# Kernel tuning notes

Hardware: AMD Instinct MI355X
Metric: run time of the kernel (lower is better)

## Reference

```python
import jax, jax.numpy as jnp
import numpy as np

N_HEAD = 16

def _rope_tables(T, hd, dtype):
    inv_freq = 1.0 / (10000.0 ** (jnp.arange(0, hd, 2, dtype=jnp.float32) / hd))
    t = jnp.arange(T, dtype=jnp.float32)
    freqs = jnp.outer(t, inv_freq)                 # [T, hd/2]
    emb = jnp.concatenate([freqs, freqs], axis=-1)  # [T, hd]
    return jnp.cos(emb).astype(dtype), jnp.sin(emb).astype(dtype)

def _rotate_half(x):
    x1, x2 = jnp.split(x, 2, axis=-1)
    return jnp.concatenate([-x2, x1], axis=-1)

def setup_inputs() -> dict:
    key = jax.random.key(0)
    ks = jax.random.split(key, 3)
    B, T, C = 2, 2048, 1024
    x = jax.random.normal(ks[0], (B, T, C), dtype=jnp.float32)
    W_attn = jax.random.normal(ks[1], (C, 3 * C), dtype=jnp.float32) * 0.02
    b_attn = jnp.zeros((3 * C,), dtype=jnp.float32)
    W_proj = jax.random.normal(ks[2], (C, C), dtype=jnp.float32) * 0.02
    b_proj = jnp.zeros((C,), dtype=jnp.float32)
    return {"x": x, "W_attn": W_attn, "b_attn": b_attn, "W_proj": W_proj, "b_proj": b_proj}

def reference(x, W_attn, b_attn, W_proj, b_proj):
    B, T, C = x.shape
    H = N_HEAD
    hd = C // H
    qkv = x @ W_attn + b_attn                       # [B,T,3C]
    q, k, v = jnp.split(qkv, 3, axis=-1)
    # [B,T,C] -> [B,H,T,hd]
    to_heads = lambda a: a.reshape(B, T, H, hd).transpose(0, 2, 1, 3)
    q, k, v = to_heads(q), to_heads(k), to_heads(v)
    cos, sin = _rope_tables(T, hd, x.dtype)         # [T,hd]
    q = q * cos + _rotate_half(q) * sin
    k = k * cos + _rotate_half(k) * sin
    scale = 1.0 / jnp.sqrt(jnp.asarray(hd, dtype=x.dtype))
    scores = jnp.einsum('bhqd,bhkd->bhqk', q, k) * scale
    causal = jnp.tril(jnp.ones((T, T), dtype=bool))
    scores = jnp.where(causal, scores, jnp.finfo(x.dtype).min)
    attn = jax.nn.softmax(scores, axis=-1)
    y = jnp.einsum('bhqk,bhkd->bhqd', attn, v)      # [B,H,T,hd]
    y = y.transpose(0, 2, 1, 3).reshape(B, T, C)
    return y @ W_proj + b_proj
```

## Files before the change

kernel.cpp:

```cpp
#include <hip/hip_runtime.h>
#include <math.h>

#define B_  2
#define T_  2048
#define C_  1024
#define H_  16
#define HD_ 64

typedef __bf16 bf16x8 __attribute__((ext_vector_type(8)));
typedef float  f32x4  __attribute__((ext_vector_type(4)));

__device__ __forceinline__ unsigned short f2bf(float f) {
    unsigned int u = __float_as_uint(f);
    unsigned int r = (u + 0x7fffu + ((u >> 16) & 1u)) >> 16;
    return (unsigned short)r;
}

__device__ __forceinline__ void async16(const void* g, void* l) {
    __builtin_amdgcn_global_load_lds(
        (const __attribute__((address_space(1))) unsigned int*)g,
        (__attribute__((address_space(3))) unsigned int*)l, 16, 0, 0);
}

__global__ __launch_bounds__(256)
void castk(const float* __restrict__ in, unsigned short* __restrict__ out, int n4)
{
    const int i = blockIdx.x * 256 + threadIdx.x;
    if (i >= n4) return;
    const float4 v = ((const float4*)in)[i];
    ushort4 o;
    o.x = f2bf(v.x); o.y = f2bf(v.y); o.z = f2bf(v.z); o.w = f2bf(v.w);
    ((ushort4*)out)[i] = o;
}

__global__ __launch_bounds__(256)
void transcast_k(const float* __restrict__ in, unsigned short* __restrict__ out,
                 int K, int N)
{
    __shared__ float t[32][33];
    const int n0 = blockIdx.x * 32, k0 = blockIdx.y * 32;
    const int tx = threadIdx.x & 31, ty = threadIdx.x >> 5;
    #pragma unroll
    for (int r = 0; r < 4; ++r)
        t[ty + 8 * r][tx] = in[(size_t)(k0 + ty + 8 * r) * N + n0 + tx];
    __syncthreads();
    #pragma unroll
    for (int r = 0; r < 4; ++r)
        out[(size_t)(n0 + ty + 8 * r) * K + k0 + tx] = f2bf(t[tx][ty + 8 * r]);
}

__global__ __launch_bounds__(256)
void rope_table_k(float2* __restrict__ tab)
{
    const int idx = blockIdx.x * 256 + threadIdx.x;
    const int dd = idx & 31;
    const int t  = idx >> 5;
    const float invf = expf(-(float)dd * (9.210340371976184f / 32.0f));
    float sn, cs;
    sincosf((float)t * invf, &sn, &cs);
    tab[idx] = make_float2(cs, sn);
}

template<int MODE>
__global__ __launch_bounds__(256)
void mgemm(const unsigned short* __restrict__ A, const unsigned short* __restrict__ Bt,
           const float* __restrict__ bias, const float2* __restrict__ rope,
           void* __restrict__ out0, void* __restrict__ out1, void* __restrict__ out2,
           int M, int N, int K)
{
    __shared__ __align__(16) unsigned short As[128 * 32];
    __shared__ __align__(16) unsigned short Bs[128 * 32];

    const int tid  = threadIdx.x;
    const int lane = tid & 63;
    const int wid  = tid >> 6;
    const int m0 = blockIdx.y * 128;
    const int n0 = blockIdx.x * 128;
    const int wr = wid >> 1, wc = wid & 1;

    const int srow = wid * 32 + (lane >> 2);
    const int scol = (lane & 3) * 8;
    const unsigned short* gA = A  + (size_t)(m0 + srow) * K + scol;
    const unsigned short* gB = Bt + (size_t)(n0 + srow) * K + scol;
    unsigned short* lA = As + wid * 1024;
    unsigned short* lB = Bs + wid * 1024;

    f32x4 acc[4][4];
    #pragma unroll
    for (int i = 0; i < 4; ++i)
        #pragma unroll
        for (int j = 0; j < 4; ++j) acc[i][j] = (f32x4)0.f;

    const int r15 = lane & 15;
    const int ko  = (lane >> 4) * 8;

    for (int kt = 0; kt < K; kt += 32) {
        __syncthreads();
        async16(gA + kt,          lA);
        async16(gA + kt + 16 * K, lA + 512);
        async16(gB + kt,          lB);
        async16(gB + kt + 16 * K, lB + 512);
        __syncthreads();

        bf16x8 af[4], bg[4];
        #pragma unroll
        for (int i = 0; i < 4; ++i)
            af[i] = *(const bf16x8*)(As + (wr * 64 + i * 16 + r15) * 32 + ko);
        #pragma unroll
        for (int j = 0; j < 4; ++j)
            bg[j] = *(const bf16x8*)(Bs + (wc * 64 + j * 16 + r15) * 32 + ko);
        #pragma unroll
        for (int i = 0; i < 4; ++i)
            #pragma unroll
            for (int j = 0; j < 4; ++j)
                acc[i][j] = __builtin_amdgcn_mfma_f32_16x16x32_bf16(af[i], bg[j], acc[i][j], 0, 0, 0);
    }

    const int rg = (lane >> 4) * 4;
    if (MODE == 0) {
        const int which = n0 >> 10;
        if (which < 2) {
            unsigned short* dst = (unsigned short*)(which == 0 ? out0 : out1);
            const int h = ((n0 & 1023) >> 6) + wc;
            #pragma unroll
            for (int i = 0; i < 4; ++i) {
                #pragma unroll
                for (int r = 0; r < 4; ++r) {
                    const int row = m0 + wr * 64 + i * 16 + rg + r;
                    const int b = row >> 11, t = row & 2047;
                    const size_t obase = (((size_t)(b * H_ + h)) * T_ + t) * HD_;
                    #pragma unroll
                    for (int j = 0; j < 2; ++j) {
                        const int d1 = j * 16 + r15;
                        const float v1 = acc[i][j][r]     + bias[n0 + wc * 64 + d1];
                        const float v2 = acc[i][j + 2][r] + bias[n0 + wc * 64 + d1 + 32];
                        const float2 cssn = rope[t * 32 + d1];
                        dst[obase + d1]      = f2bf(v1 * cssn.x - v2 * cssn.y);
                        dst[obase + d1 + 32] = f2bf(v2 * cssn.x + v1 * cssn.y);
                    }
                }
            }
        } else {
            #pragma unroll
            for (int j = 0; j < 4; ++j) {
                const int col = n0 + wc * 64 + j * 16 + r15;
                const float bv = bias[col];
                const int c = col & 1023;
                const int h = c >> 6, d = c & 63;
                #pragma unroll
                for (int i = 0; i < 4; ++i) {
                    #pragma unroll
                    for (int r = 0; r < 4; ++r) {
                        const int row = m0 + wr * 64 + i * 16 + rg + r;
                        const int b = row >> 11, t = row & 2047;
                        ((unsigned short*)out2)[(((size_t)(b * H_ + h)) * HD_ + d) * T_ + t]
                            = f2bf(acc[i][j][r] + bv);
                    }
                }
            }
        }
    } else {
        #pragma unroll
        for (int j = 0; j < 4; ++j) {
            const int col = n0 + wc * 64 + j * 16 + r15;
            const float bv = bias[col];
            #pragma unroll
            for (int i = 0; i < 4; ++i) {
                #pragma unroll
                for (int r = 0; r < 4; ++r) {
                    const int row = m0 + wr * 64 + i * 16 + rg + r;
                    ((float*)out0)[(size_t)row * N + col] = acc[i][j][r] + bv;
                }
            }
        }
    }
}

__global__ __launch_bounds__(256)
void attn_mfma(const unsigned short* __restrict__ Q,
               const unsigned short* __restrict__ K,
               const unsigned short* __restrict__ Vt,
               unsigned short* __restrict__ Y)
{
    __shared__ __align__(16) unsigned short Ks[64 * 64];
    __shared__ __align__(16) unsigned short Vs[64 * 64];
    __shared__ float Ps[4][16][68];

    const int tid  = threadIdx.x;
    const int lane = tid & 63;
    const int wid  = tid >> 6;
    const int bh   = blockIdx.x;
    const int qt   = blockIdx.y;
    const int b    = bh >> 4, h = bh & 15;
    const int g    = lane >> 4;
    const int r15  = lane & 15;
    const int sw   = (r15 & 7) << 4;

    const int srow = lane >> 3;
    const int sch  = (lane & 7) ^ srow;
    const size_t qkbase = (size_t)bh * T_ * HD_;

    const unsigned short* gK0 = K  + qkbase + (size_t)(wid * 16 + srow) * HD_ + sch * 8;
    const unsigned short* gK1 = gK0 + 8 * HD_;
    const unsigned short* gV0 = Vt + ((size_t)bh * HD_ + wid * 16 + srow) * T_ + sch * 8;
    const unsigned short* gV1 = gV0 + (size_t)8 * T_;
    unsigned short* lK0 = Ks + (wid * 16) * HD_;
    unsigned short* lK1 = lK0 + 8 * HD_;
    unsigned short* lV0 = Vs + (wid * 16) * HD_;
    unsigned short* lV1 = lV0 + 8 * HD_;

    const int qrow = qt * 64 + wid * 16 + r15;
    const unsigned short* qp = Q + qkbase + (size_t)qrow * HD_ + g * 8;
    const bf16x8 qf0 = *(const bf16x8*)(qp);
    const bf16x8 qf1 = *(const bf16x8*)(qp + 32);

    f32x4 po[4];
    float mrow[4], lrow[4];
    #pragma unroll
    for (int j = 0; j < 4; ++j) po[j] = (f32x4)0.f;
    #pragma unroll
    for (int r = 0; r < 4; ++r) { mrow[r] = -1e30f; lrow[r] = 0.f; }

    const int myrow = wid * 16 + g * 4;

    for (int kt = 0; kt <= qt; ++kt) {
        __syncthreads();
        async16(gK0 + (size_t)kt * 64 * HD_, lK0);
        async16(gK1 + (size_t)kt * 64 * HD_, lK1);
        async16(gV0 + kt * 64, lV0);
        async16(gV1 + kt * 64, lV1);
        __syncthreads();

        f32x4 sa[4];
        #pragma unroll
        for (int j = 0; j < 4; ++j) sa[j] = (f32x4)0.f;
        #pragma unroll
        for (int j = 0; j < 4; ++j) {
            const int kb0 = ((j * 16 + r15) * 128 + g * 16) ^ sw;
            const bf16x8 kf0 = *(const bf16x8*)((const char*)Ks + kb0);
            const bf16x8 kf1 = *(const bf16x8*)((const char*)Ks + (kb0 ^ 64));
            sa[j] = __builtin_amdgcn_mfma_f32_16x16x32_bf16(qf0, kf0, sa[j], 0, 0, 0);
            sa[j] = __builtin_amdgcn_mfma_f32_16x16x32_bf16(qf1, kf1, sa[j], 0, 0, 0);
        }

        const bool diag = (kt == qt);
        float p[4][4];
        #pragma unroll
        for (int r = 0; r < 4; ++r) {
            float sv[4];
            #pragma unroll
            for (int j = 0; j < 4; ++j) {
                sv[j] = sa[j][r] * 0.125f;
                if (diag && (j * 16 + r15 > myrow + r)) sv[j] = -1e30f;
            }
            float mx = fmaxf(fmaxf(sv[0], sv[1]), fmaxf(sv[2], sv[3]));
            mx = fmaxf(mx, __shfl_xor(mx, 1));
            mx = fmaxf(mx, __shfl_xor(mx, 2));
            mx = fmaxf(mx, __shfl_xor(mx, 4));
            mx = fmaxf(mx, __shfl_xor(mx, 8));
            const float mnew = fmaxf(mrow[r], mx);
            const float corr = __expf(mrow[r] - mnew);
            float rs = 0.f;
            #pragma unroll
            for (int j = 0; j < 4; ++j) {
                p[j][r] = __expf(sv[j] - mnew);
                rs += p[j][r];
            }
            rs += __shfl_xor(rs, 1);
            rs += __shfl_xor(rs, 2);
            rs += __shfl_xor(rs, 4);
            rs += __shfl_xor(rs, 8);
            lrow[r] = lrow[r] * corr + rs;
            mrow[r] = mnew;
            #pragma unroll
            for (int j2 = 0; j2 < 4; ++j2) po[j2][r] *= corr;
        }

        #pragma unroll
        for (int r = 0; r < 4; ++r)
            #pragma unroll
            for (int j = 0; j < 4; ++j)
                Ps[wid][g * 4 + r][j * 16 + r15] = p[j][r];
        union { bf16x8 v; unsigned short u[8]; } pa0, pa1;
        {
            const float4 a = *(const float4*)&Ps[wid][r15][g * 8];
            const float4 c = *(const float4*)&Ps[wid][r15][g * 8 + 4];
            pa0.u[0] = f2bf(a.x); pa0.u[1] = f2bf(a.y); pa0.u[2] = f2bf(a.z); pa0.u[3] = f2bf(a.w);
            pa0.u[4] = f2bf(c.x); pa0.u[5] = f2bf(c.y); pa0.u[6] = f2bf(c.z); pa0.u[7] = f2bf(c.w);
            const float4 d = *(const float4*)&Ps[wid][r15][32 + g * 8];
            const float4 e = *(const float4*)&Ps[wid][r15][32 + g * 8 + 4];
            pa1.u[0] = f2bf(d.x); pa1.u[1] = f2bf(d.y); pa1.u[2] = f2bf(d.z); pa1.u[3] = f2bf(d.w);
            pa1.u[4] = f2bf(e.x); pa1.u[5] = f2bf(e.y); pa1.u[6] = f2bf(e.z); pa1.u[7] = f2bf(e.w);
        }

        #pragma unroll
        for (int j2 = 0; j2 < 4; ++j2) {
            const int vb0 = ((j2 * 16 + r15) * 128 + g * 16) ^ sw;
            const bf16x8 vf0 = *(const bf16x8*)((const char*)Vs + vb0);
            const bf16x8 vf1 = *(const bf16x8*)((const char*)Vs + (vb0 ^ 64));
            po[j2] = __builtin_amdgcn_mfma_f32_16x16x32_bf16(pa0.v, vf0, po[j2], 0, 0, 0);
            po[j2] = __builtin_amdgcn_mfma_f32_16x16x32_bf16(pa1.v, vf1, po[j2], 0, 0, 0);
        }
    }

    float inv[4];
    #pragma unroll
    for (int r = 0; r < 4; ++r) inv[r] = 1.0f / lrow[r];
    #pragma unroll
    for (int j2 = 0; j2 < 4; ++j2)
        #pragma unroll
        for (int r = 0; r < 4; ++r) {
            const int t = qt * 64 + myrow + r;
            Y[((size_t)(b * T_ + t)) * C_ + h * 64 + j2 * 16 + r15] = f2bf(po[j2][r] * inv[r]);
        }
}

extern "C" void kernel_launch(void* const* d_in, const int* in_sizes, int n_in,
                              void* d_out, int out_size, void* d_ws, size_t ws_size,
                              hipStream_t stream)
{
    const float* x      = (const float*)d_in[0];
    const float* W_attn = (const float*)d_in[1];
    const float* b_attn = (const float*)d_in[2];
    const float* W_proj = (const float*)d_in[3];
    const float* b_proj = (const float*)d_in[4];
    float* out = (float*)d_out;

    const size_t NQ = (size_t)B_ * H_ * T_ * HD_;
    unsigned short* qbf = (unsigned short*)d_ws;
    unsigned short* kbf = qbf + NQ;
    unsigned short* vt  = kbf + NQ;
    unsigned short* yb  = vt  + NQ;
    unsigned short* xb  = yb  + NQ;
    unsigned short* wat = xb  + NQ;
    unsigned short* wpt = wat + (size_t)(3 * C_) * C_;
    float2* ropetab = (float2*)(wpt + (size_t)C_ * C_);

    castk<<<(int)(NQ / 4 / 256), 256, 0, stream>>>(x, xb, (int)(NQ / 4));
    transcast_k<<<dim3(3 * C_ / 32, C_ / 32), 256, 0, stream>>>(W_attn, wat, C_, 3 * C_);
    transcast_k<<<dim3(C_ / 32, C_ / 32), 256, 0, stream>>>(W_proj, wpt, C_, C_);
    rope_table_k<<<T_ * 32 / 256, 256, 0, stream>>>(ropetab);

    mgemm<0><<<dim3(3 * C_ / 128, B_ * T_ / 128), 256, 0, stream>>>(
        xb, wat, b_attn, ropetab, qbf, kbf, vt, B_ * T_, 3 * C_, C_);

    attn_mfma<<<dim3(B_ * H_, T_ / 64), 256, 0, stream>>>(qbf, kbf, vt, yb);

    mgemm<1><<<dim3(C_ / 128, B_ * T_ / 128), 256, 0, stream>>>(
        yb, wpt, b_proj, nullptr, out, nullptr, nullptr, B_ * T_, C_, C_);
}
```

Baseline: 253.5 us.

## Deepen GEMM K-tile with swizzle, prefetch K/V in registers, reorder attention tiles

```diff
diff --git a/kernel.cpp b/kernel.cpp
--- a/kernel.cpp
+++ b/kernel.cpp
@@ -68,8 +68,8 @@
            void* __restrict__ out0, void* __restrict__ out1, void* __restrict__ out2,
            int M, int N, int K)
 {
-    __shared__ __align__(16) unsigned short As[128 * 32];
-    __shared__ __align__(16) unsigned short Bs[128 * 32];
+    __shared__ __align__(16) unsigned short As[128 * 64];
+    __shared__ __align__(16) unsigned short Bs[128 * 64];
 
     const int tid  = threadIdx.x;
     const int lane = tid & 63;
@@ -78,12 +78,12 @@
     const int n0 = blockIdx.x * 128;
     const int wr = wid >> 1, wc = wid & 1;
 
-    const int srow = wid * 32 + (lane >> 2);
-    const int scol = (lane & 3) * 8;
-    const unsigned short* gA = A  + (size_t)(m0 + srow) * K + scol;
-    const unsigned short* gB = Bt + (size_t)(n0 + srow) * K + scol;
-    unsigned short* lA = As + wid * 1024;
-    unsigned short* lB = Bs + wid * 1024;
+    const int srow8 = lane >> 3;
+    const int csrc  = (lane & 7) ^ srow8;
+    const unsigned short* gA = A  + (size_t)(m0 + wid * 32 + srow8) * K + csrc * 8;
+    const unsigned short* gB = Bt + (size_t)(n0 + wid * 32 + srow8) * K + csrc * 8;
+    unsigned short* lA = As + wid * 32 * 64;
+    unsigned short* lB = Bs + wid * 32 * 64;
 
     f32x4 acc[4][4];
     #pragma unroll
@@ -92,31 +92,41 @@
         for (int j = 0; j < 4; ++j) acc[i][j] = (f32x4)0.f;
 
     const int r15 = lane & 15;
-    const int ko  = (lane >> 4) * 8;
-
-    for (int kt = 0; kt < K; kt += 32) {
+    const int g   = lane >> 4;
+    const int sw  = (r15 & 7) << 4;
+
+    for (int kt = 0; kt < K; kt += 64) {
         __syncthreads();
         async16(gA + kt,          lA);
-        async16(gA + kt + 16 * K, lA + 512);
+        async16(gA + kt +  8 * K, lA + 512);
+        async16(gA + kt + 16 * K, lA + 1024);
+        async16(gA + kt + 24 * K, lA + 1536);
         async16(gB + kt,          lB);
-        async16(gB + kt + 16 * K, lB + 512);
+        async16(gB + kt +  8 * K, lB + 512);
+        async16(gB + kt + 16 * K, lB + 1024);
+        async16(gB + kt + 24 * K, lB + 1536);
         __syncthreads();
 
-        bf16x8 af[4], bg[4];
-        #pragma unroll
-        for (int i = 0; i < 4; ++i)
-            af[i] = *(const bf16x8*)(As + (wr * 64 + i * 16 + r15) * 32 + ko);
-        #pragma unroll
-        for (int j = 0; j < 4; ++j)
-            bg[j] = *(const bf16x8*)(Bs + (wc * 64 + j * 16 + r15) * 32 + ko);
-        #pragma unroll
-        for (int i = 0; i < 4; ++i)
+        #pragma unroll
+        for (int kk = 0; kk < 2; ++kk) {
+            bf16x8 af[4], bg[4];
+            #pragma unroll
+            for (int i = 0; i < 4; ++i)
+                af[i] = *(const bf16x8*)((const char*)As +
+                        ((((wr * 64 + i * 16 + r15) << 7) + (kk << 6) + (g << 4)) ^ sw));
             #pragma unroll
             for (int j = 0; j < 4; ++j)
-                acc[i][j] = __builtin_amdgcn_mfma_f32_16x16x32_bf16(af[i], bg[j], acc[i][j], 0, 0, 0);
+                bg[j] = *(const bf16x8*)((const char*)Bs +
+                        ((((wc * 64 + j * 16 + r15) << 7) + (kk << 6) + (g << 4)) ^ sw));
+            #pragma unroll
+            for (int i = 0; i < 4; ++i)
+                #pragma unroll
+                for (int j = 0; j < 4; ++j)
+                    acc[i][j] = __builtin_amdgcn_mfma_f32_16x16x32_bf16(af[i], bg[j], acc[i][j], 0, 0, 0);
+        }
     }
 
-    const int rg = (lane >> 4) * 4;
+    const int rg = g * 4;
     if (MODE == 0) {
         const int which = n0 >> 10;
         if (which < 2) {
@@ -190,24 +200,25 @@
     const int lane = tid & 63;
     const int wid  = tid >> 6;
     const int bh   = blockIdx.x;
-    const int qt   = blockIdx.y;
+    const int y    = blockIdx.y;
+    const int y0   = y & 7;
+    const int yk   = y >> 3;
+    const int qt   = (yk == 0) ? y0 : (yk == 1) ? (15 - y0)
+                   : (yk == 2) ? (16 + y0) : (31 - y0);
     const int b    = bh >> 4, h = bh & 15;
     const int g    = lane >> 4;
     const int r15  = lane & 15;
     const int sw   = (r15 & 7) << 4;
 
-    const int srow = lane >> 3;
-    const int sch  = (lane & 7) ^ srow;
+    const int srow8 = lane >> 3;
+    const int c8    = lane & 7;
+    const int wsw   = (c8 ^ srow8) << 4;
+
     const size_t qkbase = (size_t)bh * T_ * HD_;
-
-    const unsigned short* gK0 = K  + qkbase + (size_t)(wid * 16 + srow) * HD_ + sch * 8;
-    const unsigned short* gK1 = gK0 + 8 * HD_;
-    const unsigned short* gV0 = Vt + ((size_t)bh * HD_ + wid * 16 + srow) * T_ + sch * 8;
-    const unsigned short* gV1 = gV0 + (size_t)8 * T_;
-    unsigned short* lK0 = Ks + (wid * 16) * HD_;
-    unsigned short* lK1 = lK0 + 8 * HD_;
-    unsigned short* lV0 = Vs + (wid * 16) * HD_;
-    unsigned short* lV1 = lV0 + 8 * HD_;
+    const unsigned short* gK = K  + qkbase + (size_t)(wid * 16 + srow8) * HD_ + c8 * 8;
+    const unsigned short* gV = Vt + ((size_t)bh * HD_ + wid * 16 + srow8) * T_ + c8 * 8;
+    char* lK = (char*)Ks + (wid * 16 + srow8) * 128 + wsw;
+    char* lV = (char*)Vs + (wid * 16 + srow8) * 128 + wsw;
 
     const int qrow = qt * 64 + wid * 16 + r15;
     const unsigned short* qp = Q + qkbase + (size_t)qrow * HD_ + g * 8;
@@ -222,14 +233,27 @@
     for (int r = 0; r < 4; ++r) { mrow[r] = -1e30f; lrow[r] = 0.f; }
 
     const int myrow = wid * 16 + g * 4;
+    const float C2 = 0.18033688011112042f;
+
+    uint4 kr0 = *(const uint4*)(gK);
+    uint4 kr1 = *(const uint4*)(gK + 8 * HD_);
+    uint4 vr0 = *(const uint4*)(gV);
+    uint4 vr1 = *(const uint4*)(gV + 8 * T_);
 
     for (int kt = 0; kt <= qt; ++kt) {
+        *(uint4*)(lK)           = kr0;
+        *(uint4*)(lK + 8 * 128) = kr1;
+        *(uint4*)(lV)           = vr0;
+        *(uint4*)(lV + 8 * 128) = vr1;
         __syncthreads();
-        async16(gK0 + (size_t)kt * 64 * HD_, lK0);
-        async16(gK1 + (size_t)kt * 64 * HD_, lK1);
-        async16(gV0 + kt * 64, lV0);
-        async16(gV1 + kt * 64, lV1);
-        __syncthreads();
+
+        if (kt < qt) {
+            const size_t ko = (size_t)(kt + 1) * 64;
+            kr0 = *(const uint4*)(gK + ko * HD_);
+            kr1 = *(const uint4*)(gK + ko * HD_ + 8 * HD_);
+            vr0 = *(const uint4*)(gV + ko);
+            vr1 = *(const uint4*)(gV + ko + 8 * T_);
+        }
 
         f32x4 sa[4];
         #pragma unroll
@@ -247,23 +271,25 @@
         float p[4][4];
         #pragma unroll
         for (int r = 0; r < 4; ++r) {
-            float sv[4];
-            #pragma unroll
-            for (int j = 0; j < 4; ++j) {
-                sv[j] = sa[j][r] * 0.125f;
-                if (diag && (j * 16 + r15 > myrow + r)) sv[j] = -1e30f;
-            }
-            float mx = fmaxf(fmaxf(sv[0], sv[1]), fmaxf(sv[2], sv[3]));
+            float sc[4];
+            #pragma unroll
+            for (int j = 0; j < 4; ++j) sc[j] = sa[j][r] * C2;
+            if (diag) {
+                #pragma unroll
+                for (int j = 0; j < 4; ++j)
+                    if (j * 16 + r15 > myrow + r) sc[j] = -1e30f;
+            }
+            float mx = fmaxf(fmaxf(sc[0], sc[1]), fmaxf(sc[2], sc[3]));
             mx = fmaxf(mx, __shfl_xor(mx, 1));
             mx = fmaxf(mx, __shfl_xor(mx, 2));
             mx = fmaxf(mx, __shfl_xor(mx, 4));
             mx = fmaxf(mx, __shfl_xor(mx, 8));
             const float mnew = fmaxf(mrow[r], mx);
-            const float corr = __expf(mrow[r] - mnew);
+            const float corr = exp2f(mrow[r] - mnew);
             float rs = 0.f;
             #pragma unroll
             for (int j = 0; j < 4; ++j) {
-                p[j][r] = __expf(sv[j] - mnew);
+                p[j][r] = exp2f(sc[j] - mnew);
                 rs += p[j][r];
             }
             rs += __shfl_xor(rs, 1);
@@ -301,6 +327,8 @@
             po[j2] = __builtin_amdgcn_mfma_f32_16x16x32_bf16(pa0.v, vf0, po[j2], 0, 0, 0);
             po[j2] = __builtin_amdgcn_mfma_f32_16x16x32_bf16(pa1.v, vf1, po[j2], 0, 0, 0);
         }
+
+        __syncthreads();
     }
 
     float inv[4];
```

After: 237.9 us. 1.07x faster.
